# Kernel optimization log

Hardware: AMD Instinct MI355X
Metric: run time of the kernel (lower is better)

Reference implementation:

```python
import jax, jax.numpy as jnp
import numpy as np

B, D, U = 4096, 2048, 2048

def setup_inputs() -> dict:
    key = jax.random.key(0)
    ks = jax.random.split(key, 16)
    s_in = 1.0 / np.sqrt(D)
    s_h = 1.0 / np.sqrt(U)
    inp = {
        "x": jax.random.normal(ks[0], (B, D), jnp.float32),
        "h": jax.random.normal(ks[1], (B, U), jnp.float32),
        "c": jax.random.normal(ks[2], (B, U), jnp.float32),
        # input-to-gate weights (Dense with bias)
        "Wxf": jax.random.normal(ks[3], (D, U), jnp.float32) * s_in,
        "Wxi": jax.random.normal(ks[4], (D, U), jnp.float32) * s_in,
        "Wxo": jax.random.normal(ks[5], (D, U), jnp.float32) * s_in,
        "Wxg": jax.random.normal(ks[6], (D, U), jnp.float32) * s_in,
        "bf": jnp.zeros((U,), jnp.float32),
        "bi": jnp.zeros((U,), jnp.float32),
        "bo": jnp.zeros((U,), jnp.float32),
        "bg": jnp.zeros((U,), jnp.float32),
        # hidden-to-gate weights (no bias)
        "Whf": jax.random.normal(ks[7], (U, U), jnp.float32) * s_h,
        "Whi": jax.random.normal(ks[8], (U, U), jnp.float32) * s_h,
        "Who": jax.random.normal(ks[9], (U, U), jnp.float32) * s_h,
        "Whg": jax.random.normal(ks[10], (U, U), jnp.float32) * s_h,
    }
    return inp

def reference(x, h, c, Wxf, Wxi, Wxo, Wxg, bf, bi, bo, bg, Whf, Whi, Who, Whg):
    # Fuse the 8 small GEMMs into two batched GEMMs over concatenated weights,
    # then one elementwise gate-fusion pass. Math identical to per-Dense form.
    Wx = jnp.concatenate([Wxf, Wxi, Wxo, Wxg], axis=1)   # [D, 4U]
    Wh = jnp.concatenate([Whf, Whi, Who, Whg], axis=1)   # [U, 4U]
    b = jnp.concatenate([bf, bi, bo, bg], axis=0)        # [4U]
    z = x @ Wx + h @ Wh + b                               # [B, 4U]
    zf, zi, zo, zg = jnp.split(z, 4, axis=1)
    f = jax.nn.sigmoid(zf)
    i = jax.nn.sigmoid(zi)
    o = jax.nn.sigmoid(zo)
    g = jnp.tanh(zg)
    c_new = f * c + i * g
    h_new = o * jnp.tanh(c_new)
    return (h_new, c_new)
```

## Files before the change

### kernel.cpp

```cpp
#include <hip/hip_runtime.h>
#include <hip/hip_bf16.h>
#include <stdint.h>

#define B_ 4096
#define D_ 2048
#define U_ 2048
#define K_ 4096
#define N_ 8192

typedef __bf16 bf16x8 __attribute__((ext_vector_type(8)));
typedef float floatx4 __attribute__((ext_vector_type(4)));
typedef unsigned short ushort8 __attribute__((ext_vector_type(8)));

__device__ __forceinline__ unsigned short f2bf(float f) {
    union { float f; unsigned int u; } v; v.f = f;
    unsigned int u = v.u;
    unsigned int r = (u + 0x7fffu + ((u >> 16) & 1u)) >> 16;
    return (unsigned short)r;
}

__device__ __forceinline__ float bf2f(unsigned short b) {
    union { unsigned int u; float f; } v;
    v.u = ((unsigned int)b) << 16;
    return v.f;
}

__device__ __forceinline__ float sigmoid_(float x) {
    return 1.0f / (1.0f + __expf(-x));
}
__device__ __forceinline__ float tanh_(float x) {
    return 1.0f - 2.0f / (__expf(2.0f * x) + 1.0f);
}

__global__ void k_convA(const float* __restrict__ x, const float* __restrict__ h,
                        unsigned short* __restrict__ Abf) {
    int t = blockIdx.x * blockDim.x + threadIdx.x;
    long e = (long)t * 4;
    int b = (int)(e >> 12);
    int k = (int)(e & 4095);
    const float* src = (k < D_) ? (x + (size_t)b * D_ + k)
                                : (h + (size_t)b * U_ + (k - D_));
    float4 v = *(const float4*)src;
    ushort4 o;
    o.x = f2bf(v.x); o.y = f2bf(v.y); o.z = f2bf(v.z); o.w = f2bf(v.w);
    *(ushort4*)(Abf + e) = o;
}

__global__ __launch_bounds__(256) void k_convB(
        const float* __restrict__ Wx0, const float* __restrict__ Wx1,
        const float* __restrict__ Wx2, const float* __restrict__ Wx3,
        const float* __restrict__ Wh0, const float* __restrict__ Wh1,
        const float* __restrict__ Wh2, const float* __restrict__ Wh3,
        unsigned short* __restrict__ Bt) {
    __shared__ float tile[64][65];
    const int g  = blockIdx.z;
    const int k0 = blockIdx.x * 64;
    const int u0 = blockIdx.y * 64;
    const int t  = threadIdx.x;
    const float* W;
    if (k0 < D_) {
        W = (g == 0 ? Wx0 : g == 1 ? Wx1 : g == 2 ? Wx2 : Wx3) + (size_t)k0 * U_;
    } else {
        W = (g == 0 ? Wh0 : g == 1 ? Wh1 : g == 2 ? Wh2 : Wh3) + (size_t)(k0 - D_) * U_;
    }
    {
        const int kr_b = t >> 4;
        const int uc   = (t & 15) * 4;
        #pragma unroll
        for (int p = 0; p < 4; ++p) {
            int kr = p * 16 + kr_b;
            float4 v = *(const float4*)(W + (size_t)kr * U_ + u0 + uc);
            tile[kr][uc + 0] = v.x;
            tile[kr][uc + 1] = v.y;
            tile[kr][uc + 2] = v.z;
            tile[kr][uc + 3] = v.w;
        }
    }
    __syncthreads();
    {
        const int kc = (t & 7) * 8;
        #pragma unroll
        for (int p = 0; p < 2; ++p) {
            int u_idx = p * 32 + (t >> 3);
            int u = u0 + u_idx;
            int nrow = g * U_ + u;
            ushort8 o;
            #pragma unroll
            for (int kk = 0; kk < 8; ++kk)
                o[kk] = f2bf(tile[kc + kk][u_idx]);
            *(ushort8*)(Bt + (size_t)nrow * K_ + k0 + kc) = o;
        }
    }
}

__device__ __forceinline__ void gload16(const unsigned short* g, unsigned short* l) {
    __builtin_amdgcn_global_load_lds(
        (const __attribute__((address_space(1))) void*)g,
        (__attribute__((address_space(3))) void*)l, 16, 0, 0);
}

#define BARRIER() __builtin_amdgcn_s_barrier()

__global__ __launch_bounds__(512, 2) void k_gemm(const unsigned short* __restrict__ A,
                                                 const unsigned short* __restrict__ Bt,
                                                 unsigned short* __restrict__ Z) {
    __shared__ __align__(16) unsigned short sm[3 * 16384];

    const int id  = blockIdx.x;
    const int swz = (id & 7) * 64 + (id >> 3);
    const int m0  = (swz & 15) << 8;
    const int n0  = (swz >> 4) << 8;

    const int tid  = threadIdx.x;
    const int w    = tid >> 6;
    const int l    = tid & 63;
    const int wr   = w >> 2;
    const int wc   = w & 3;
    const int r    = l & 15;
    const int quad = l >> 4;
    const int sw8  = (quad ^ ((r >> 1) & 3)) << 3;

    const int aBase = (wr * 128 + r) * 32 + sw8;
    const int bBase = 8192 + (wc * 64 + r) * 32 + sw8;

    const int srow = tid >> 2;
    const int sg   = (((tid & 3) ^ ((srow >> 1) & 3)) << 3);
    const unsigned short* gA0 = A  + (size_t)(m0 + srow      ) * K_ + sg;
    const unsigned short* gA1 = A  + (size_t)(m0 + 128 + srow) * K_ + sg;
    const unsigned short* gB0 = Bt + (size_t)(n0 + srow      ) * K_ + sg;
    const unsigned short* gB1 = Bt + (size_t)(n0 + 128 + srow) * K_ + sg;
    unsigned short* const stw = sm + w * 512;

    floatx4 acc[8][4];
    #pragma unroll
    for (int i = 0; i < 8; ++i)
        #pragma unroll
        for (int j = 0; j < 4; ++j)
            #pragma unroll
            for (int e = 0; e < 4; ++e) acc[i][j][e] = 0.f;

    #pragma unroll
    for (int tt = 0; tt < 2; ++tt) {
        unsigned short* b = stw + tt * 16384;
        const int kt = tt * 32;
        gload16(gA0 + kt, b);
        gload16(gA1 + kt, b + 4096);
        gload16(gB0 + kt, b + 8192);
        gload16(gB1 + kt, b + 12288);
    }
    asm volatile("s_waitcnt vmcnt(4)" ::: "memory");
    BARRIER();

    int c = 0;
    for (int t = 0; t < 128; ++t) {
        const unsigned short* Sb = sm + c * 16384;
        const int cst = (c == 0) ? 2 : c - 1;
        unsigned short* sb = stw + cst * 16384;
        const int kt = (t + 2) * 32;
        const bool st = (t < 126);

        bf16x8 bq[4], aq[8];
        #pragma unroll
        for (int j = 0; j < 4; ++j) bq[j] = *(const bf16x8*)(Sb + bBase + j * 512);
        #pragma unroll
        for (int i = 0; i < 8; ++i) aq[i] = *(const bf16x8*)(Sb + aBase + i * 512);
        if (st) {
            gload16(gA0 + kt, sb);
            gload16(gA1 + kt, sb + 4096);
            gload16(gB0 + kt, sb + 8192);
            gload16(gB1 + kt, sb + 12288);
        }
        __builtin_amdgcn_s_setprio(1);
        #pragma unroll
        for (int i = 0; i < 8; ++i)
            #pragma unroll
            for (int j = 0; j < 4; ++j)
                acc[i][j] = __builtin_amdgcn_mfma_f32_16x16x32_bf16(
                    aq[i], bq[j], acc[i][j], 0, 0, 0);
        __builtin_amdgcn_s_setprio(0);
        if (st) asm volatile("s_waitcnt vmcnt(4)" ::: "memory");
        else    asm volatile("s_waitcnt vmcnt(0)" ::: "memory");
        BARRIER();

        c = (c == 2) ? 0 : c + 1;
    }

    #pragma unroll
    for (int i = 0; i < 8; ++i) {
        #pragma unroll
        for (int j = 0; j < 4; ++j) {
            const int col = n0 + wc * 64 + j * 16 + r;
            #pragma unroll
            for (int e = 0; e < 4; ++e) {
                const int row = m0 + wr * 128 + i * 16 + quad * 4 + e;
                Z[(size_t)row * N_ + col] = f2bf(acc[i][j][e]);
            }
        }
    }
}

__global__ void k_gates(const unsigned short* __restrict__ Z, const float* __restrict__ c,
                        const float* __restrict__ bfp, const float* __restrict__ bip,
                        const float* __restrict__ bop, const float* __restrict__ bgp,
                        float* __restrict__ hout, float* __restrict__ cout) {
    int t = blockIdx.x * blockDim.x + threadIdx.x;
    long e = (long)t * 4;
    int b = (int)(e >> 11);
    int u = (int)(e & 2047);
    const size_t zr = (size_t)b * N_;
    ushort4 zf4 = *(const ushort4*)(Z + zr + u);
    ushort4 zi4 = *(const ushort4*)(Z + zr + U_ + u);
    ushort4 zo4 = *(const ushort4*)(Z + zr + 2 * U_ + u);
    ushort4 zg4 = *(const ushort4*)(Z + zr + 3 * U_ + u);
    float4 bfv = *(const float4*)(bfp + u);
    float4 biv = *(const float4*)(bip + u);
    float4 bov = *(const float4*)(bop + u);
    float4 bgv = *(const float4*)(bgp + u);
    float4 cv  = *(const float4*)(c + e);

    float zf[4] = {bf2f(zf4.x), bf2f(zf4.y), bf2f(zf4.z), bf2f(zf4.w)};
    float zi[4] = {bf2f(zi4.x), bf2f(zi4.y), bf2f(zi4.z), bf2f(zi4.w)};
    float zo[4] = {bf2f(zo4.x), bf2f(zo4.y), bf2f(zo4.z), bf2f(zo4.w)};
    float zg[4] = {bf2f(zg4.x), bf2f(zg4.y), bf2f(zg4.z), bf2f(zg4.w)};
    float bff[4] = {bfv.x, bfv.y, bfv.z, bfv.w};
    float bif[4] = {biv.x, biv.y, biv.z, biv.w};
    float bof[4] = {bov.x, bov.y, bov.z, bov.w};
    float bgf[4] = {bgv.x, bgv.y, bgv.z, bgv.w};
    float cf[4]  = {cv.x, cv.y, cv.z, cv.w};

    float hh[4], cc[4];
    #pragma unroll
    for (int q = 0; q < 4; ++q) {
        float f = sigmoid_(zf[q] + bff[q]);
        float i = sigmoid_(zi[q] + bif[q]);
        float o = sigmoid_(zo[q] + bof[q]);
        float g = tanh_(zg[q] + bgf[q]);
        float cn = f * cf[q] + i * g;
        cc[q] = cn;
        hh[q] = o * tanh_(cn);
    }
    float4 ho, co;
    ho.x = hh[0]; ho.y = hh[1]; ho.z = hh[2]; ho.w = hh[3];
    co.x = cc[0]; co.y = cc[1]; co.z = cc[2]; co.w = cc[3];
    *(float4*)(hout + e) = ho;
    *(float4*)(cout + e) = co;
}

extern "C" void kernel_launch(void* const* d_in, const int* in_sizes, int n_in,
                              void* d_out, int out_size, void* d_ws, size_t ws_size,
                              hipStream_t stream) {
    const float* x   = (const float*)d_in[0];
    const float* h   = (const float*)d_in[1];
    const float* c   = (const float*)d_in[2];
    const float* Wxf = (const float*)d_in[3];
    const float* Wxi = (const float*)d_in[4];
    const float* Wxo = (const float*)d_in[5];
    const float* Wxg = (const float*)d_in[6];
    const float* bf  = (const float*)d_in[7];
    const float* bi  = (const float*)d_in[8];
    const float* bo  = (const float*)d_in[9];
    const float* bg  = (const float*)d_in[10];
    const float* Whf = (const float*)d_in[11];
    const float* Whi = (const float*)d_in[12];
    const float* Who = (const float*)d_in[13];
    const float* Whg = (const float*)d_in[14];
    float* out = (float*)d_out;

    unsigned short* Abf = (unsigned short*)d_ws;
    unsigned short* Bt  = Abf + (size_t)B_ * K_;
    unsigned short* Z   = Bt + (size_t)N_ * K_;

    k_convA<<<(B_ * K_ / 4) / 256, 256, 0, stream>>>(x, h, Abf);
    k_convB<<<dim3(K_ / 64, U_ / 64, 4), 256, 0, stream>>>(
        Wxf, Wxi, Wxo, Wxg, Whf, Whi, Who, Whg, Bt);
    k_gemm<<<dim3((B_ / 256) * (N_ / 256)), 512, 0, stream>>>(Abf, Bt, Z);
    k_gates<<<(B_ * U_ / 4) / 256, 256, 0, stream>>>(
        Z, c, bf, bi, bo, bg, out, out + (size_t)B_ * U_);
}
```

Baseline: 503.9 us.

## Switch GEMM to double-buffered LDS with register fragment ping-pong

The GEMM main loop moves from a three-stage LDS ring to two LDS buffers plus two register sets of A/B fragments. While the MFMAs run on one fragment set, the next tile is loaded from LDS and the tile after that is fetched from global memory. Fixed sched_group_barrier hints pin the ordering of MFMA and LDS reads. Cutting shared memory per block is meant to raise occupancy and hide LDS latency behind MFMAs. In exchange, the loop waits for all global loads (vmcnt 0) every half-iteration, and the second fragment set adds register pressure.

```diff
diff --git a/kernel.cpp b/kernel.cpp
--- a/kernel.cpp
+++ b/kernel.cpp
@@ -101,10 +101,44 @@
 
 #define BARRIER() __builtin_amdgcn_s_barrier()
 
+#define STAGE(BUFBASE, KT) do { \
+    gload16(gA0 + (KT), (BUFBASE)); \
+    gload16(gA1 + (KT), (BUFBASE) + 4096); \
+    gload16(gB0 + (KT), (BUFBASE) + 8192); \
+    gload16(gB1 + (KT), (BUFBASE) + 12288); \
+} while (0)
+
+#define READ_FRAGS(SBASE, AQ, BQ) do { \
+    _Pragma("unroll") \
+    for (int j_ = 0; j_ < 4; ++j_) BQ[j_] = *(const bf16x8*)((SBASE) + bBase + j_ * 512); \
+    _Pragma("unroll") \
+    for (int i_ = 0; i_ < 8; ++i_) AQ[i_] = *(const bf16x8*)((SBASE) + aBase + i_ * 512); \
+} while (0)
+
+#define MFMA_ALL(AQ, BQ) do { \
+    _Pragma("unroll") \
+    for (int i_ = 0; i_ < 8; ++i_) \
+        _Pragma("unroll") \
+        for (int j_ = 0; j_ < 4; ++j_) \
+            acc[i_][j_] = __builtin_amdgcn_mfma_f32_16x16x32_bf16( \
+                AQ[i_], BQ[j_], acc[i_][j_], 0, 0, 0); \
+} while (0)
+
+#define PIN_SCHED() do { \
+    __builtin_amdgcn_sched_group_barrier(0x100, 12, 0);  \
+    __builtin_amdgcn_sched_group_barrier(0x008, 32, 0);  \
+} while (0)
+
+#define BODY_WAITS() do { \
+    asm volatile("s_waitcnt lgkmcnt(0)" ::: "memory"); \
+    asm volatile("s_waitcnt vmcnt(0)" ::: "memory"); \
+    BARRIER(); \
+} while (0)
+
 __global__ __launch_bounds__(512, 2) void k_gemm(const unsigned short* __restrict__ A,
                                                  const unsigned short* __restrict__ Bt,
                                                  unsigned short* __restrict__ Z) {
-    __shared__ __align__(16) unsigned short sm[3 * 16384];
+    __shared__ __align__(16) unsigned short sm[2 * 16384];
 
     const int id  = blockIdx.x;
     const int swz = (id & 7) * 64 + (id >> 3);
@@ -129,7 +163,10 @@
     const unsigned short* gA1 = A  + (size_t)(m0 + 128 + srow) * K_ + sg;
     const unsigned short* gB0 = Bt + (size_t)(n0 + srow      ) * K_ + sg;
     const unsigned short* gB1 = Bt + (size_t)(n0 + 128 + srow) * K_ + sg;
-    unsigned short* const stw = sm + w * 512;
+    unsigned short* const stw0 = sm + w * 512;
+    unsigned short* const stw1 = sm + 16384 + w * 512;
+    const unsigned short* const Sb0 = sm;
+    const unsigned short* const Sb1 = sm + 16384;
 
     floatx4 acc[8][4];
     #pragma unroll
@@ -139,51 +176,39 @@
             #pragma unroll
             for (int e = 0; e < 4; ++e) acc[i][j][e] = 0.f;
 
-    #pragma unroll
-    for (int tt = 0; tt < 2; ++tt) {
-        unsigned short* b = stw + tt * 16384;
-        const int kt = tt * 32;
-        gload16(gA0 + kt, b);
-        gload16(gA1 + kt, b + 4096);
-        gload16(gB0 + kt, b + 8192);
-        gload16(gB1 + kt, b + 12288);
-    }
-    asm volatile("s_waitcnt vmcnt(4)" ::: "memory");
+    bf16x8 aqA[8], bqA[4], aqB[8], bqB[4];
+
+    STAGE(stw0, 0);
+    STAGE(stw1, 32);
+    asm volatile("s_waitcnt vmcnt(0)" ::: "memory");
     BARRIER();
-
-    int c = 0;
-    for (int t = 0; t < 128; ++t) {
-        const unsigned short* Sb = sm + c * 16384;
-        const int cst = (c == 0) ? 2 : c - 1;
-        unsigned short* sb = stw + cst * 16384;
-        const int kt = (t + 2) * 32;
-        const bool st = (t < 126);
-
-        bf16x8 bq[4], aq[8];
-        #pragma unroll
-        for (int j = 0; j < 4; ++j) bq[j] = *(const bf16x8*)(Sb + bBase + j * 512);
-        #pragma unroll
-        for (int i = 0; i < 8; ++i) aq[i] = *(const bf16x8*)(Sb + aBase + i * 512);
-        if (st) {
-            gload16(gA0 + kt, sb);
-            gload16(gA1 + kt, sb + 4096);
-            gload16(gB0 + kt, sb + 8192);
-            gload16(gB1 + kt, sb + 12288);
-        }
+    READ_FRAGS(Sb0, aqA, bqA);
+    asm volatile("s_waitcnt lgkmcnt(0)" ::: "memory");
+    BARRIER();
+
+    for (int tt = 0; tt < 63; ++tt) {
+        STAGE(stw0, 64 * tt + 64);
+        READ_FRAGS(Sb1, aqB, bqB);
         __builtin_amdgcn_s_setprio(1);
-        #pragma unroll
-        for (int i = 0; i < 8; ++i)
-            #pragma unroll
-            for (int j = 0; j < 4; ++j)
-                acc[i][j] = __builtin_amdgcn_mfma_f32_16x16x32_bf16(
-                    aq[i], bq[j], acc[i][j], 0, 0, 0);
+        MFMA_ALL(aqA, bqA);
         __builtin_amdgcn_s_setprio(0);
-        if (st) asm volatile("s_waitcnt vmcnt(4)" ::: "memory");
-        else    asm volatile("s_waitcnt vmcnt(0)" ::: "memory");
-        BARRIER();
-
-        c = (c == 2) ? 0 : c + 1;
-    }
+        PIN_SCHED();
+        BODY_WAITS();
+
+        STAGE(stw1, 64 * tt + 96);
+        READ_FRAGS(Sb0, aqA, bqA);
+        __builtin_amdgcn_s_setprio(1);
+        MFMA_ALL(aqB, bqB);
+        __builtin_amdgcn_s_setprio(0);
+        PIN_SCHED();
+        BODY_WAITS();
+    }
+
+    READ_FRAGS(Sb1, aqB, bqB);
+    __builtin_amdgcn_s_setprio(1);
+    MFMA_ALL(aqA, bqA);
+    MFMA_ALL(aqB, bqB);
+    __builtin_amdgcn_s_setprio(0);
 
     #pragma unroll
     for (int i = 0; i < 8; ++i) {
```

Result: slower. 520.5 us (+3.3%).

## Fuse LSTM gate epilogue into GEMM by interleaving gate columns per tile

Applied to the files above, without the earlier changes.

Each GEMM tile now covers 64 hidden units across all four gates: the B-tile rows are gathered from the f/i/o/g column blocks, so every thread holds all four gate pre-activations for the same (row, unit). The sigmoid/tanh cell update runs directly in the GEMM epilogue, which removes the bf16 Z intermediate and the separate gates kernel. This saves the round trip of writing and re-reading Z and one launch, and keeps the pre-activations in fp32 instead of rounding them to bf16. The cost is that the epilogue stores are scattered 4-byte writes with stride along rows, and the heavier epilogue adds work inside the GEMM kernel.

```diff
diff --git a/kernel.cpp b/kernel.cpp
--- a/kernel.cpp
+++ b/kernel.cpp
@@ -17,12 +17,6 @@
     unsigned int u = v.u;
     unsigned int r = (u + 0x7fffu + ((u >> 16) & 1u)) >> 16;
     return (unsigned short)r;
-}
-
-__device__ __forceinline__ float bf2f(unsigned short b) {
-    union { unsigned int u; float f; } v;
-    v.u = ((unsigned int)b) << 16;
-    return v.f;
 }
 
 __device__ __forceinline__ float sigmoid_(float x) {
@@ -103,13 +97,19 @@
 
 __global__ __launch_bounds__(512, 2) void k_gemm(const unsigned short* __restrict__ A,
                                                  const unsigned short* __restrict__ Bt,
-                                                 unsigned short* __restrict__ Z) {
+                                                 const float* __restrict__ cvec,
+                                                 const float* __restrict__ bfp,
+                                                 const float* __restrict__ bip,
+                                                 const float* __restrict__ bop,
+                                                 const float* __restrict__ bgp,
+                                                 float* __restrict__ hout,
+                                                 float* __restrict__ cout) {
     __shared__ __align__(16) unsigned short sm[3 * 16384];
 
     const int id  = blockIdx.x;
     const int swz = (id & 7) * 64 + (id >> 3);
     const int m0  = (swz & 15) << 8;
-    const int n0  = (swz >> 4) << 8;
+    const int u0  = (swz >> 4) << 6;
 
     const int tid  = threadIdx.x;
     const int w    = tid >> 6;
@@ -121,14 +121,14 @@
     const int sw8  = (quad ^ ((r >> 1) & 3)) << 3;
 
     const int aBase = (wr * 128 + r) * 32 + sw8;
-    const int bBase = 8192 + (wc * 64 + r) * 32 + sw8;
+    const int bBase = 8192 + (wc * 16 + r) * 32 + sw8;
 
     const int srow = tid >> 2;
     const int sg   = (((tid & 3) ^ ((srow >> 1) & 3)) << 3);
-    const unsigned short* gA0 = A  + (size_t)(m0 + srow      ) * K_ + sg;
-    const unsigned short* gA1 = A  + (size_t)(m0 + 128 + srow) * K_ + sg;
-    const unsigned short* gB0 = Bt + (size_t)(n0 + srow      ) * K_ + sg;
-    const unsigned short* gB1 = Bt + (size_t)(n0 + 128 + srow) * K_ + sg;
+    const unsigned short* gA0 = A + (size_t)(m0 + srow      ) * K_ + sg;
+    const unsigned short* gA1 = A + (size_t)(m0 + 128 + srow) * K_ + sg;
+    const unsigned short* gB0 = Bt + (size_t)(((srow >> 6)    ) * U_ + u0 + (srow & 63)) * K_ + sg;
+    const unsigned short* gB1 = Bt + (size_t)(((srow >> 6) + 2) * U_ + u0 + (srow & 63)) * K_ + sg;
     unsigned short* const stw = sm + w * 512;
 
     floatx4 acc[8][4];
@@ -161,7 +161,7 @@
 
         bf16x8 bq[4], aq[8];
         #pragma unroll
-        for (int j = 0; j < 4; ++j) bq[j] = *(const bf16x8*)(Sb + bBase + j * 512);
+        for (int j = 0; j < 4; ++j) bq[j] = *(const bf16x8*)(Sb + bBase + j * 2048);
         #pragma unroll
         for (int i = 0; i < 8; ++i) aq[i] = *(const bf16x8*)(Sb + aBase + i * 512);
         if (st) {
@@ -185,65 +185,23 @@
         c = (c == 2) ? 0 : c + 1;
     }
 
+    const int u = u0 + wc * 16 + r;
+    const float bfv = bfp[u], biv = bip[u], bov = bop[u], bgv = bgp[u];
     #pragma unroll
     for (int i = 0; i < 8; ++i) {
         #pragma unroll
-        for (int j = 0; j < 4; ++j) {
-            const int col = n0 + wc * 64 + j * 16 + r;
-            #pragma unroll
-            for (int e = 0; e < 4; ++e) {
-                const int row = m0 + wr * 128 + i * 16 + quad * 4 + e;
-                Z[(size_t)row * N_ + col] = f2bf(acc[i][j][e]);
-            }
-        }
-    }
-}
-
-__global__ void k_gates(const unsigned short* __restrict__ Z, const float* __restrict__ c,
-                        const float* __restrict__ bfp, const float* __restrict__ bip,
-                        const float* __restrict__ bop, const float* __restrict__ bgp,
-                        float* __restrict__ hout, float* __restrict__ cout) {
-    int t = blockIdx.x * blockDim.x + threadIdx.x;
-    long e = (long)t * 4;
-    int b = (int)(e >> 11);
-    int u = (int)(e & 2047);
-    const size_t zr = (size_t)b * N_;
-    ushort4 zf4 = *(const ushort4*)(Z + zr + u);
-    ushort4 zi4 = *(const ushort4*)(Z + zr + U_ + u);
-    ushort4 zo4 = *(const ushort4*)(Z + zr + 2 * U_ + u);
-    ushort4 zg4 = *(const ushort4*)(Z + zr + 3 * U_ + u);
-    float4 bfv = *(const float4*)(bfp + u);
-    float4 biv = *(const float4*)(bip + u);
-    float4 bov = *(const float4*)(bop + u);
-    float4 bgv = *(const float4*)(bgp + u);
-    float4 cv  = *(const float4*)(c + e);
-
-    float zf[4] = {bf2f(zf4.x), bf2f(zf4.y), bf2f(zf4.z), bf2f(zf4.w)};
-    float zi[4] = {bf2f(zi4.x), bf2f(zi4.y), bf2f(zi4.z), bf2f(zi4.w)};
-    float zo[4] = {bf2f(zo4.x), bf2f(zo4.y), bf2f(zo4.z), bf2f(zo4.w)};
-    float zg[4] = {bf2f(zg4.x), bf2f(zg4.y), bf2f(zg4.z), bf2f(zg4.w)};
-    float bff[4] = {bfv.x, bfv.y, bfv.z, bfv.w};
-    float bif[4] = {biv.x, biv.y, biv.z, biv.w};
-    float bof[4] = {bov.x, bov.y, bov.z, bov.w};
-    float bgf[4] = {bgv.x, bgv.y, bgv.z, bgv.w};
-    float cf[4]  = {cv.x, cv.y, cv.z, cv.w};
-
-    float hh[4], cc[4];
-    #pragma unroll
-    for (int q = 0; q < 4; ++q) {
-        float f = sigmoid_(zf[q] + bff[q]);
-        float i = sigmoid_(zi[q] + bif[q]);
-        float o = sigmoid_(zo[q] + bof[q]);
-        float g = tanh_(zg[q] + bgf[q]);
-        float cn = f * cf[q] + i * g;
-        cc[q] = cn;
-        hh[q] = o * tanh_(cn);
-    }
-    float4 ho, co;
-    ho.x = hh[0]; ho.y = hh[1]; ho.z = hh[2]; ho.w = hh[3];
-    co.x = cc[0]; co.y = cc[1]; co.z = cc[2]; co.w = cc[3];
-    *(float4*)(hout + e) = ho;
-    *(float4*)(cout + e) = co;
+        for (int e = 0; e < 4; ++e) {
+            const int row = m0 + wr * 128 + i * 16 + quad * 4 + e;
+            const size_t cu = (size_t)row * U_ + u;
+            float f  = sigmoid_(acc[i][0][e] + bfv);
+            float ig = sigmoid_(acc[i][1][e] + biv);
+            float o  = sigmoid_(acc[i][2][e] + bov);
+            float g  = tanh_(acc[i][3][e] + bgv);
+            float cn = f * cvec[cu] + ig * g;
+            hout[cu] = o * tanh_(cn);
+            cout[cu] = cn;
+        }
+    }
 }
 
 extern "C" void kernel_launch(void* const* d_in, const int* in_sizes, int n_in,
@@ -268,12 +226,10 @@
 
     unsigned short* Abf = (unsigned short*)d_ws;
     unsigned short* Bt  = Abf + (size_t)B_ * K_;
-    unsigned short* Z   = Bt + (size_t)N_ * K_;
 
     k_convA<<<(B_ * K_ / 4) / 256, 256, 0, stream>>>(x, h, Abf);
     k_convB<<<dim3(K_ / 64, U_ / 64, 4), 256, 0, stream>>>(
         Wxf, Wxi, Wxo, Wxg, Whf, Whi, Who, Whg, Bt);
-    k_gemm<<<dim3((B_ / 256) * (N_ / 256)), 512, 0, stream>>>(Abf, Bt, Z);
-    k_gates<<<(B_ * U_ / 4) / 256, 256, 0, stream>>>(
-        Z, c, bf, bi, bo, bg, out, out + (size_t)B_ * U_);
-}
+    k_gemm<<<dim3((B_ / 256) * (U_ / 64)), 512, 0, stream>>>(
+        Abf, Bt, c, bf, bi, bo, bg, out, out + (size_t)B_ * U_);
+}
```

Result: faster. 493.8 us (-2.0%).
